# Kernel tuning notes

Measured on AMD Instinct MI355X. Metric: run time of the kernel, lower is better.

The kernel has to match this reference:

```python
import jax, jax.numpy as jnp
import numpy as np

N_HEADS = 16
N_KV_HEADS = 8
DIM = 2048
HEAD_DIM = DIM // N_HEADS  # 128
N_REP = N_HEADS // N_KV_HEADS


def _rope(t, cos, sin):
    # t: [B, S, H, D]; cos/sin: [S, D//2]
    t2 = t.reshape(*t.shape[:-1], -1, 2)  # [B,S,H,D/2,2]
    p1, p2 = t2[..., 0], t2[..., 1]
    c = cos[None, :, None, :]
    s = sin[None, :, None, :]
    r1 = p1 * c - p2 * s
    r2 = p1 * s + p2 * c
    return jnp.stack((r1, r2), axis=-1).reshape(t.shape)


def setup_inputs() -> dict:
    key = jax.random.key(0)
    ks = jax.random.split(key, 7)
    B, S = 2, 2048
    x = jax.random.normal(ks[0], (B, S, DIM), dtype=jnp.float32)
    freqs_cos = jax.random.normal(ks[1], (S, HEAD_DIM // 2), dtype=jnp.float32)
    freqs_sin = jax.random.normal(ks[2], (S, HEAD_DIM // 2), dtype=jnp.float32)
    sc = 1.0 / np.sqrt(DIM)
    wq = jax.random.normal(ks[3], (DIM, N_HEADS * HEAD_DIM), dtype=jnp.float32) * sc
    wk = jax.random.normal(ks[4], (DIM, N_KV_HEADS * HEAD_DIM), dtype=jnp.float32) * sc
    wv = jax.random.normal(ks[5], (DIM, N_KV_HEADS * HEAD_DIM), dtype=jnp.float32) * sc
    wo = jax.random.normal(ks[6], (N_HEADS * HEAD_DIM, DIM), dtype=jnp.float32) * sc
    return {"x": x, "freqs_cos": freqs_cos, "freqs_sin": freqs_sin,
            "wq": wq, "wk": wk, "wv": wv, "wo": wo}


def reference(x, freqs_cos, freqs_sin, wq, wk, wv, wo):
    B, S, _ = x.shape
    xq = (x @ wq).reshape(B, S, N_HEADS, HEAD_DIM)
    xk = (x @ wk).reshape(B, S, N_KV_HEADS, HEAD_DIM)
    xv = (x @ wv).reshape(B, S, N_KV_HEADS, HEAD_DIM)
    xq = _rope(xq, freqs_cos, freqs_sin)
    xk = _rope(xk, freqs_cos, freqs_sin)
    # GQA repeat_kv: [B,S,Hkv,D] -> [B,S,Hkv*n_rep,D]
    xk = jnp.repeat(xk, N_REP, axis=2)
    xv = jnp.repeat(xv, N_REP, axis=2)
    q = xq.transpose(0, 2, 1, 3)  # [B,H,S,D]
    k = xk.transpose(0, 2, 1, 3)
    v = xv.transpose(0, 2, 1, 3)
    scale = 1.0 / np.sqrt(HEAD_DIM)
    scores = jnp.einsum('bhqd,bhkd->bhqk', q, k) * scale
    causal = jnp.tril(jnp.ones((S, S), dtype=bool))
    scores = jnp.where(causal[None, None], scores, -jnp.inf)
    probs = jax.nn.softmax(scores.astype(jnp.float32), axis=-1).astype(q.dtype)
    out = jnp.einsum('bhqk,bhkd->bhqd', probs, v)
    out = out.transpose(0, 2, 1, 3).reshape(B, S, N_HEADS * HEAD_DIM)
    return out @ wo
```

## Files before the change

### kernel.cpp

```cpp
#include <hip/hip_runtime.h>
#include <cstdint>
#include <cstddef>

#define S_LEN 2048
#define DIM_   2048
#define NH   16
#define NKV  8
#define HD   128

typedef __attribute__((ext_vector_type(8))) __bf16 bf16x8;
typedef __attribute__((ext_vector_type(4))) float  f32x4;

typedef const __attribute__((address_space(1))) void* gptr_t;
typedef __attribute__((address_space(3))) void*       sptr_t;

static __device__ __forceinline__ float bf2f(unsigned short u) {
  union { unsigned int i; float f; } v; v.i = ((unsigned int)u) << 16; return v.f;
}
static __device__ __forceinline__ unsigned short f2bf(float f) {
  union { float f; unsigned int i; } v; v.f = f;
  unsigned int u = v.i;
  unsigned int r = (u + 0x7FFFu + ((u >> 16) & 1u)) >> 16;
  return (unsigned short)r;
}

#define QSCALE 0.12751744f
#define RESC_THR 11.542f

__global__ void k_prep(const float* __restrict__ x, unsigned short* __restrict__ xb,
                       const float* __restrict__ wq, const float* __restrict__ wk,
                       const float* __restrict__ wv, const float* __restrict__ wo,
                       unsigned short* __restrict__ wqkvT, unsigned short* __restrict__ woT) {
  int bid = blockIdx.x;
  if (bid < 8192) {
    int i = bid * 256 + threadIdx.x;
    float4 v = ((const float4*)x)[i];
    ushort4 o; o.x = f2bf(v.x); o.y = f2bf(v.y); o.z = f2bf(v.z); o.w = f2bf(v.w);
    ((ushort4*)xb)[i] = o;
    return;
  }
  bid -= 8192;
  const float* src; unsigned short* dst; int N, ntx;
  if (bid < 4096)      { src = wq; dst = wqkvT;                       N = 2048; ntx = 64; }
  else if (bid < 6144) { bid -= 4096; src = wk; dst = wqkvT + (size_t)2048 * 2048; N = 1024; ntx = 32; }
  else if (bid < 8192) { bid -= 6144; src = wv; dst = wqkvT + (size_t)3072 * 2048; N = 1024; ntx = 32; }
  else                 { bid -= 8192; src = wo; dst = woT;            N = 2048; ntx = 64; }
  const int K = 2048;
  __shared__ float tile[32][33];
  int lx = threadIdx.x & 31, ly = threadIdx.x >> 5;
  int r0 = (bid / ntx) * 32, c0 = (bid % ntx) * 32;
  #pragma unroll
  for (int r = 0; r < 32; r += 8)
    tile[ly + r][lx] = src[(size_t)(r0 + ly + r) * N + c0 + lx];
  __syncthreads();
  #pragma unroll
  for (int r = 0; r < 32; r += 8)
    dst[(size_t)(c0 + ly + r) * K + r0 + lx] = f2bf(tile[lx][ly + r]);
}

template<int MODE>
__global__ __launch_bounds__(256, 2) void k_gemm_bt(
    const unsigned short* __restrict__ A, const unsigned short* __restrict__ BT,
    void* __restrict__ C, int N, int K,
    const float* __restrict__ fc, const float* __restrict__ fs,
    unsigned short* __restrict__ kb, unsigned short* __restrict__ vb) {
  __shared__ __align__(16) unsigned short Asm[128 * 64];
  __shared__ __align__(16) unsigned short Bsm[128 * 64];
  const int t = threadIdx.x;
  const int lane = t & 63, w = t >> 6;
  const int wm = (w >> 1) * 64, wn = (w & 1) * 64;
  const int col = lane & 15, quad = lane >> 4;
  const int m0 = blockIdx.y * 128, n0 = blockIdx.x * 128;

  f32x4 acc[4][4];
  #pragma unroll
  for (int i = 0; i < 4; i++)
    #pragma unroll
    for (int j = 0; j < 4; j++) acc[i][j] = (f32x4){0.f, 0.f, 0.f, 0.f};

  for (int kk = 0; kk < K; kk += 64) {
    #pragma unroll
    for (int r = 0; r < 4; ++r) {
      int c = t + r * 256;
      int c0 = (t & ~63) + r * 256;
      int row = c >> 3;
      int kcs = (c & 7) ^ (row & 7);
      const unsigned short* gA = A + (size_t)(m0 + row) * K + kk + kcs * 8;
      const unsigned short* gB = BT + (size_t)(n0 + row) * K + kk + kcs * 8;
      __builtin_amdgcn_global_load_lds((gptr_t)gA, (sptr_t)(&Asm[c0 * 8]), 16, 0, 0);
      __builtin_amdgcn_global_load_lds((gptr_t)gB, (sptr_t)(&Bsm[c0 * 8]), 16, 0, 0);
    }
    __syncthreads();
    #pragma unroll
    for (int kc2 = 0; kc2 < 2; kc2++) {
      bf16x8 af[4], bf[4];
      #pragma unroll
      for (int mi = 0; mi < 4; mi++) {
        int rowA = wm + mi * 16 + col;
        af[mi] = *(const bf16x8*)(&Asm[rowA * 64 + (((kc2 * 4 + quad) ^ (col & 7)) * 8)]);
      }
      #pragma unroll
      for (int ni = 0; ni < 4; ni++) {
        int rowB = wn + ni * 16 + col;
        bf[ni] = *(const bf16x8*)(&Bsm[rowB * 64 + (((kc2 * 4 + quad) ^ (col & 7)) * 8)]);
      }
      #pragma unroll
      for (int mi = 0; mi < 4; mi++)
        #pragma unroll
        for (int ni = 0; ni < 4; ni++)
          acc[mi][ni] = __builtin_amdgcn_mfma_f32_16x16x32_bf16(af[mi], bf[ni], acc[mi][ni], 0, 0, 0);
    }
    __syncthreads();
  }

  #pragma unroll
  for (int mi = 0; mi < 4; mi++) {
    int row_base = m0 + wm + mi * 16 + quad * 4;
    #pragma unroll
    for (int ni = 0; ni < 4; ni++) {
      int col_g = n0 + wn + ni * 16 + col;
      if (MODE == 1) {
        float* O = (float*)C;
        #pragma unroll
        for (int r = 0; r < 4; r++) O[(size_t)(row_base + r) * N + col_g] = acc[mi][ni][r];
      } else {
        int region = col_g >> 10;
        if (region < 3) {
          int ri = (col_g & 127) >> 1;
          float sgn = (col_g & 1) ? 1.f : -1.f;
          unsigned short* qO = (unsigned short*)C;
          #pragma unroll
          for (int r = 0; r < 4; r++) {
            int row = row_base + r;
            int s = row & (S_LEN - 1);
            float cv = fc[s * 64 + ri], sv = fs[s * 64 + ri];
            float val = acc[mi][ni][r];
            float other = __shfl_xor(val, 1);
            float res = val * cv + sgn * other * sv;
            if (region < 2) qO[(size_t)row * 2048 + col_g] = f2bf(res * QSCALE);
            else            kb[(size_t)row * 1024 + (col_g - 2048)] = f2bf(res);
          }
        } else {
          int n_local = col_g - 3072;
          int b = row_base >> 11, s = row_base & (S_LEN - 1);
          int kvh = n_local >> 7, d = n_local & (HD - 1);
          ushort4 o4;
          o4.x = f2bf(acc[mi][ni][0]); o4.y = f2bf(acc[mi][ni][1]);
          o4.z = f2bf(acc[mi][ni][2]); o4.w = f2bf(acc[mi][ni][3]);
          *(ushort4*)(&vb[((size_t)((b * NKV + kvh) * HD + d)) * S_LEN + s]) = o4;
        }
      }
    }
  }
}

#define KLD 136
#define VLD 72
__global__ __launch_bounds__(512, 2) void k_attn(
    const unsigned short* __restrict__ q, const unsigned short* __restrict__ k,
    const unsigned short* __restrict__ vT, unsigned short* __restrict__ ao) {
  __shared__ __align__(16) unsigned short Ksm[64 * KLD];
  __shared__ __align__(16) unsigned short Vsm[128 * VLD];
  __shared__ __align__(16) unsigned short Psm[8 * 16 * VLD];
  const int t = threadIdx.x;
  const int lane = t & 63, w = t >> 6;
  const int col = lane & 15, quad = lane >> 4;
  const int g = blockIdx.x;
  const int b = g >> 3, kvh = g & 7;
  const int h = kvh * 2 + (w >> 2);
  const int yi = blockIdx.y;
  const int my_qt = (yi < 16) ? yi : 47 - yi;
  const int qrow = my_qt * 64 + (w & 3) * 16;
  unsigned short* Pw = &Psm[w * 16 * VLD];

  const int ki0 = t >> 4,        kdc = t & 15;
  const int ki1 = (t + 512) >> 4;
  const int vd0 = t >> 3,        vkc = t & 7;
  const int vd1 = (t + 512) >> 3;
  const unsigned short* kgp = k + (size_t)(b * S_LEN) * (NKV * HD) + kvh * HD + kdc * 8;
  const unsigned short* vgp = vT + ((size_t)(b * NKV + kvh) * HD) * S_LEN + vkc * 8;

  bf16x8 qf[4];
  const size_t qbase = ((size_t)(b * S_LEN) + qrow + col) * DIM_ + h * HD;
  #pragma unroll
  for (int kc = 0; kc < 4; kc++) qf[kc] = *(const bf16x8*)(q + qbase + kc * 32 + quad * 8);

  f32x4 o[8];
  #pragma unroll
  for (int i = 0; i < 8; i++) o[i] = (f32x4){0.f, 0.f, 0.f, 0.f};
  float m_i = -1e30f;
  float l_i = 0.f;

  const int nkt = my_qt + 1;

  {
    uint4 kr0 = *(const uint4*)(kgp + (size_t)ki0 * (NKV * HD));
    uint4 kr1 = *(const uint4*)(kgp + (size_t)ki1 * (NKV * HD));
    uint4 vr0 = *(const uint4*)(vgp + (size_t)vd0 * S_LEN);
    uint4 vr1 = *(const uint4*)(vgp + (size_t)vd1 * S_LEN);
    *(uint4*)(&Ksm[ki0 * KLD + kdc * 8]) = kr0;
    *(uint4*)(&Ksm[ki1 * KLD + kdc * 8]) = kr1;
    *(uint4*)(&Vsm[vd0 * VLD + vkc * 8]) = vr0;
    *(uint4*)(&Vsm[vd1 * VLD + vkc * 8]) = vr1;
  }
  __syncthreads();

  for (int kt = 0; kt < nkt; ++kt) {
    const bool more = (kt + 1 < nkt);
    uint4 kr0, kr1, vr0, vr1;
    if (more) {
      kr0 = *(const uint4*)(kgp + (size_t)((kt + 1) * 64 + ki0) * (NKV * HD));
      kr1 = *(const uint4*)(kgp + (size_t)((kt + 1) * 64 + ki1) * (NKV * HD));
    }

    float p[4][4];
    __builtin_amdgcn_s_setprio(1);
    #pragma unroll
    for (int nt = 0; nt < 4; nt++) {
      f32x4 s_acc = (f32x4){0.f, 0.f, 0.f, 0.f};
      #pragma unroll
      for (int kc = 0; kc < 4; kc++) {
        bf16x8 kf = *(const bf16x8*)(&Ksm[(nt * 16 + col) * KLD + kc * 32 + quad * 8]);
        s_acc = __builtin_amdgcn_mfma_f32_16x16x32_bf16(kf, qf[kc], s_acc, 0, 0, 0);
      }
      #pragma unroll
      for (int r = 0; r < 4; r++) p[nt][r] = s_acc[r];
    }
    __builtin_amdgcn_s_setprio(0);

    if (kt == my_qt) {
      const int qglob = qrow + col;
      #pragma unroll
      for (int nt = 0; nt < 4; nt++)
        #pragma unroll
        for (int r = 0; r < 4; r++)
          if (kt * 64 + nt * 16 + quad * 4 + r > qglob) p[nt][r] = -1e30f;
    }

    float mx = fmaxf(fmaxf(fmaxf(p[0][0], p[0][1]), fmaxf(p[0][2], p[0][3])),
                     fmaxf(fmaxf(p[1][0], p[1][1]), fmaxf(p[1][2], p[1][3])));
    mx = fmaxf(mx, fmaxf(fmaxf(fmaxf(p[2][0], p[2][1]), fmaxf(p[2][2], p[2][3])),
                         fmaxf(fmaxf(p[3][0], p[3][1]), fmaxf(p[3][2], p[3][3]))));
    mx = fmaxf(mx, __shfl_xor(mx, 16));
    mx = fmaxf(mx, __shfl_xor(mx, 32));
    if (__any(mx - m_i > RESC_THR)) {
      float mn = fmaxf(m_i, mx);
      float alpha = exp2f(m_i - mn);
      m_i = mn; l_i *= alpha;
      float ar[4];
      #pragma unroll
      for (int r = 0; r < 4; r++) ar[r] = __shfl(alpha, quad * 4 + r);
      #pragma unroll
      for (int dt = 0; dt < 8; dt++)
        #pragma unroll
        for (int r = 0; r < 4; r++) o[dt][r] *= ar[r];
    }
    float rs = 0.f;
    #pragma unroll
    for (int nt = 0; nt < 4; nt++)
      #pragma unroll
      for (int r = 0; r < 4; r++) {
        float e = exp2f(p[nt][r] - m_i);
        p[nt][r] = e;
        rs += e;
      }
    rs += __shfl_xor(rs, 16);
    rs += __shfl_xor(rs, 32);
    l_i += rs;

    #pragma unroll
    for (int nt = 0; nt < 4; nt++) {
      unsigned int w0 = (unsigned int)f2bf(p[nt][0]) | ((unsigned int)f2bf(p[nt][1]) << 16);
      unsigned int w1 = (unsigned int)f2bf(p[nt][2]) | ((unsigned int)f2bf(p[nt][3]) << 16);
      uint2 pk; pk.x = w0; pk.y = w1;
      *(uint2*)(&Pw[col * VLD + nt * 16 + quad * 4]) = pk;
    }

    __syncthreads();

    if (more) {
      *(uint4*)(&Ksm[ki0 * KLD + kdc * 8]) = kr0;
      *(uint4*)(&Ksm[ki1 * KLD + kdc * 8]) = kr1;
      vr0 = *(const uint4*)(vgp + (size_t)vd0 * S_LEN + (kt + 1) * 64);
      vr1 = *(const uint4*)(vgp + (size_t)vd1 * S_LEN + (kt + 1) * 64);
    }

    bf16x8 pf[2];
    #pragma unroll
    for (int kc2 = 0; kc2 < 2; kc2++)
      pf[kc2] = *(const bf16x8*)(&Pw[col * VLD + kc2 * 32 + quad * 8]);

    __builtin_amdgcn_s_setprio(1);
    #pragma unroll
    for (int dt = 0; dt < 8; dt++) {
      #pragma unroll
      for (int kc2 = 0; kc2 < 2; kc2++) {
        bf16x8 vf = *(const bf16x8*)(&Vsm[(dt * 16 + col) * VLD + kc2 * 32 + quad * 8]);
        o[dt] = __builtin_amdgcn_mfma_f32_16x16x32_bf16(pf[kc2], vf, o[dt], 0, 0, 0);
      }
    }
    __builtin_amdgcn_s_setprio(0);

    __syncthreads();

    if (more) {
      *(uint4*)(&Vsm[vd0 * VLD + vkc * 8]) = vr0;
      *(uint4*)(&Vsm[vd1 * VLD + vkc * 8]) = vr1;
    }
  }

  float linv[4];
  #pragma unroll
  for (int r = 0; r < 4; r++) linv[r] = 1.f / __shfl(l_i, quad * 4 + r);
  #pragma unroll
  for (int dt = 0; dt < 8; dt++) {
    int dcol = h * HD + dt * 16 + col;
    #pragma unroll
    for (int r = 0; r < 4; r++) {
      int rg = qrow + quad * 4 + r;
      ao[((size_t)(b * S_LEN) + rg) * DIM_ + dcol] = f2bf(o[dt][r] * linv[r]);
    }
  }
}

extern "C" void kernel_launch(void* const* d_in, const int* in_sizes, int n_in,
                              void* d_out, int out_size, void* d_ws, size_t ws_size,
                              hipStream_t stream) {
  const float* x  = (const float*)d_in[0];
  const float* fc = (const float*)d_in[1];
  const float* fs = (const float*)d_in[2];
  const float* wq = (const float*)d_in[3];
  const float* wk = (const float*)d_in[4];
  const float* wv = (const float*)d_in[5];
  const float* wo = (const float*)d_in[6];
  float* out = (float*)d_out;

  char* ws = (char*)d_ws;
  const size_t MB = 1024 * 1024;
  unsigned short* xb    = (unsigned short*)(ws + 0 * MB);
  unsigned short* wqkvT = (unsigned short*)(ws + 16 * MB);
  unsigned short* woT   = (unsigned short*)(ws + 32 * MB);
  unsigned short* qb    = (unsigned short*)(ws + 40 * MB);
  unsigned short* kb    = (unsigned short*)(ws + 56 * MB);
  unsigned short* vT    = (unsigned short*)(ws + 64 * MB);
  unsigned short* ao    = (unsigned short*)(ws + 72 * MB);

  k_prep<<<dim3(20480), dim3(256), 0, stream>>>(x, xb, wq, wk, wv, wo, wqkvT, woT);
  k_gemm_bt<3><<<dim3(32, 32), dim3(256), 0, stream>>>(xb, wqkvT, (void*)qb, 4096, 2048, fc, fs, kb, vT);
  k_attn<<<dim3(16, 32), dim3(512), 0, stream>>>(qb, kb, vT, ao);
  k_gemm_bt<1><<<dim3(16, 32), dim3(256), 0, stream>>>(ao, woT, (void*)out, 2048, 2048, nullptr, nullptr, nullptr, nullptr);
}
```

Before: 335.9 us.

## Replace GEMM with 256-wide tiles and a 4-stage async LDS pipeline

Rewrites the bf16 GEMM kernel to use 512-thread blocks with 256x256 (QKV) or 128x256 (output projection) tiles. It adds a 4-deep ring of LDS buffers fed by global_load_lds three tiles ahead, with explicit vmcnt waits and a single barrier per k-step. A new row-paired swizzle is used, and s_setprio is raised around the MFMA block. The intent is to hide global load latency and raise arithmetic intensity per block. The cost is higher register and LDS pressure, one block per CU, and fewer blocks, which can leave CUs idle on the output projection (256 blocks).

Result: slower. 372.0 us (+10.8%).

```diff
diff --git a/kernel.cpp b/kernel.cpp
--- a/kernel.cpp
+++ b/kernel.cpp
@@ -58,63 +58,95 @@
     dst[(size_t)(c0 + ly + r) * K + r0 + lx] = f2bf(tile[lx][ly + r]);
 }
 
-template<int MODE>
-__global__ __launch_bounds__(256, 2) void k_gemm_bt(
+template<int MODE, int BM_>
+__global__ __launch_bounds__(512, 1) void k_gemm256(
     const unsigned short* __restrict__ A, const unsigned short* __restrict__ BT,
     void* __restrict__ C, int N, int K,
     const float* __restrict__ fc, const float* __restrict__ fs,
     unsigned short* __restrict__ kb, unsigned short* __restrict__ vb) {
-  __shared__ __align__(16) unsigned short Asm[128 * 64];
-  __shared__ __align__(16) unsigned short Bsm[128 * 64];
+  constexpr int MI = BM_ / 32;
+  constexpr int AR = BM_ / 128;
+  __shared__ __align__(16) unsigned short Abuf[4][BM_ * 32];
+  __shared__ __align__(16) unsigned short Bbuf[4][256 * 32];
   const int t = threadIdx.x;
   const int lane = t & 63, w = t >> 6;
-  const int wm = (w >> 1) * 64, wn = (w & 1) * 64;
   const int col = lane & 15, quad = lane >> 4;
-  const int m0 = blockIdx.y * 128, n0 = blockIdx.x * 128;
-
-  f32x4 acc[4][4];
-  #pragma unroll
-  for (int i = 0; i < 4; i++)
+  const int wm = (w >> 2) * (BM_ / 2);
+  const int wn = (w & 3) * 64;
+  const int m0 = blockIdx.y * BM_, n0 = blockIdx.x * 256;
+  const int NT = K >> 5;
+
+  size_t srcA[2], srcB[2];
+  int ldsoff[2];
+  #pragma unroll
+  for (int r = 0; r < 2; ++r) {
+    int c = t + r * 512;
+    int row = (c >> 3) * 2 + ((c >> 2) & 1);
+    int ch  = (c & 3) ^ ((c >> 3) & 3);
+    srcA[r] = (r < AR) ? ((size_t)(m0 + row) * K + ch * 8) : 0;
+    srcB[r] = (size_t)(n0 + row) * K + ch * 8;
+    ldsoff[r] = (w * 64 + r * 512) * 8;
+  }
+
+  f32x4 acc[MI][4];
+  #pragma unroll
+  for (int i = 0; i < MI; i++)
     #pragma unroll
     for (int j = 0; j < 4; j++) acc[i][j] = (f32x4){0.f, 0.f, 0.f, 0.f};
 
-  for (int kk = 0; kk < K; kk += 64) {
-    #pragma unroll
-    for (int r = 0; r < 4; ++r) {
-      int c = t + r * 256;
-      int c0 = (t & ~63) + r * 256;
-      int row = c >> 3;
-      int kcs = (c & 7) ^ (row & 7);
-      const unsigned short* gA = A + (size_t)(m0 + row) * K + kk + kcs * 8;
-      const unsigned short* gB = BT + (size_t)(n0 + row) * K + kk + kcs * 8;
-      __builtin_amdgcn_global_load_lds((gptr_t)gA, (sptr_t)(&Asm[c0 * 8]), 16, 0, 0);
-      __builtin_amdgcn_global_load_lds((gptr_t)gB, (sptr_t)(&Bsm[c0 * 8]), 16, 0, 0);
-    }
-    __syncthreads();
-    #pragma unroll
-    for (int kc2 = 0; kc2 < 2; kc2++) {
-      bf16x8 af[4], bf[4];
-      #pragma unroll
-      for (int mi = 0; mi < 4; mi++) {
-        int rowA = wm + mi * 16 + col;
-        af[mi] = *(const bf16x8*)(&Asm[rowA * 64 + (((kc2 * 4 + quad) ^ (col & 7)) * 8)]);
-      }
-      #pragma unroll
-      for (int ni = 0; ni < 4; ni++) {
-        int rowB = wn + ni * 16 + col;
-        bf[ni] = *(const bf16x8*)(&Bsm[rowB * 64 + (((kc2 * 4 + quad) ^ (col & 7)) * 8)]);
-      }
-      #pragma unroll
-      for (int mi = 0; mi < 4; mi++)
-        #pragma unroll
-        for (int ni = 0; ni < 4; ni++)
-          acc[mi][ni] = __builtin_amdgcn_mfma_f32_16x16x32_bf16(af[mi], bf[ni], acc[mi][ni], 0, 0, 0);
-    }
-    __syncthreads();
-  }
-
-  #pragma unroll
-  for (int mi = 0; mi < 4; mi++) {
+  #define ISSUE_TILE(T)                                                              \
+    do {                                                                             \
+      int _buf = (T) & 3;                                                            \
+      _Pragma("unroll")                                                              \
+      for (int r = 0; r < AR; ++r)                                                   \
+        __builtin_amdgcn_global_load_lds((gptr_t)(A + srcA[r] + (size_t)(T) * 32),   \
+            (sptr_t)(&Abuf[_buf][ldsoff[r]]), 16, 0, 0);                             \
+      _Pragma("unroll")                                                              \
+      for (int r = 0; r < 2; ++r)                                                    \
+        __builtin_amdgcn_global_load_lds((gptr_t)(BT + srcB[r] + (size_t)(T) * 32),  \
+            (sptr_t)(&Bbuf[_buf][ldsoff[r]]), 16, 0, 0);                             \
+    } while (0)
+
+  ISSUE_TILE(0); ISSUE_TILE(1); ISSUE_TILE(2);
+
+  for (int kt = 0; kt < NT; ++kt) {
+    if constexpr (BM_ == 256) {
+      if (kt < NT - 2)       asm volatile("s_waitcnt vmcnt(8)" ::: "memory");
+      else if (kt == NT - 2) asm volatile("s_waitcnt vmcnt(4)" ::: "memory");
+      else                   asm volatile("s_waitcnt vmcnt(0)" ::: "memory");
+    } else {
+      if (kt < NT - 2)       asm volatile("s_waitcnt vmcnt(6)" ::: "memory");
+      else if (kt == NT - 2) asm volatile("s_waitcnt vmcnt(3)" ::: "memory");
+      else                   asm volatile("s_waitcnt vmcnt(0)" ::: "memory");
+    }
+    __builtin_amdgcn_s_barrier();
+    asm volatile("" ::: "memory");
+    if (kt + 3 < NT) ISSUE_TILE(kt + 3);
+
+    const int buf = kt & 3;
+    bf16x8 bfr[4], afr[MI];
+    #pragma unroll
+    for (int ni = 0; ni < 4; ni++) {
+      int row = wn + ni * 16 + col;
+      bfr[ni] = *(const bf16x8*)(&Bbuf[buf][(row >> 1) * 64 + (row & 1) * 32 + ((quad ^ ((row >> 1) & 3)) * 8)]);
+    }
+    #pragma unroll
+    for (int mi = 0; mi < MI; mi++) {
+      int row = wm + mi * 16 + col;
+      afr[mi] = *(const bf16x8*)(&Abuf[buf][(row >> 1) * 64 + (row & 1) * 32 + ((quad ^ ((row >> 1) & 3)) * 8)]);
+    }
+    __builtin_amdgcn_s_setprio(1);
+    #pragma unroll
+    for (int mi = 0; mi < MI; mi++)
+      #pragma unroll
+      for (int ni = 0; ni < 4; ni++)
+        acc[mi][ni] = __builtin_amdgcn_mfma_f32_16x16x32_bf16(afr[mi], bfr[ni], acc[mi][ni], 0, 0, 0);
+    __builtin_amdgcn_s_setprio(0);
+  }
+  #undef ISSUE_TILE
+
+  #pragma unroll
+  for (int mi = 0; mi < MI; mi++) {
     int row_base = m0 + wm + mi * 16 + quad * 4;
     #pragma unroll
     for (int ni = 0; ni < 4; ni++) {
@@ -346,7 +378,7 @@
   unsigned short* ao    = (unsigned short*)(ws + 72 * MB);
 
   k_prep<<<dim3(20480), dim3(256), 0, stream>>>(x, xb, wq, wk, wv, wo, wqkvT, woT);
-  k_gemm_bt<3><<<dim3(32, 32), dim3(256), 0, stream>>>(xb, wqkvT, (void*)qb, 4096, 2048, fc, fs, kb, vT);
+  k_gemm256<3, 256><<<dim3(16, 16), dim3(512), 0, stream>>>(xb, wqkvT, (void*)qb, 4096, 2048, fc, fs, kb, vT);
   k_attn<<<dim3(16, 32), dim3(512), 0, stream>>>(qb, kb, vT, ao);
-  k_gemm_bt<1><<<dim3(16, 32), dim3(256), 0, stream>>>(ao, woT, (void*)out, 2048, 2048, nullptr, nullptr, nullptr, nullptr);
-}
+  k_gemm256<1, 128><<<dim3(8, 32), dim3(512), 0, stream>>>(ao, woT, (void*)out, 2048, 2048, nullptr, nullptr, nullptr, nullptr);
+}
```
